# Performance work log

Measured on AMD Instinct MI355X. Metric: run time of the kernel, lower is better.

Reference implementation:

```python
import jax, jax.numpy as jnp
import numpy as np

B, H, S, D = 2, 8, 2048, 64
TEMPERATURE = 8.0  # sqrt(D)

def setup_inputs() -> dict:
    key = jax.random.key(0)
    k1, k2, k3, k4, k5 = jax.random.split(key, 5)
    q = jax.random.normal(k1, (B, H, S, D), dtype=jnp.float32)
    k = jax.random.normal(k2, (B, H, S, D), dtype=jnp.float32)
    v = jax.random.normal(k3, (B, H, S, D), dtype=jnp.float32)
    static_cov = jax.random.normal(k4, (B, S, S), dtype=jnp.float32)
    mask = jax.random.randint(k5, (B, 1, S, S), 0, 2, dtype=jnp.int32)
    # learned parameter: lambda_w initialized to 10 per head, shape [1,H,1,1]
    lambda_w = jnp.full((1, H, 1, 1), 10.0, dtype=jnp.float32)
    return {"q": q, "k": k, "v": v, "static_cov": static_cov,
            "lambda_w": lambda_w, "mask": mask}

def reference(q, k, v, static_cov, lambda_w, mask):
    # blend of scaled QK^T and static covariance bias, convex weights per head
    w_qk = 1.0 / (lambda_w + 1.0)          # [1,H,1,1]
    w_cov = lambda_w / (lambda_w + 1.0)    # [1,H,1,1]
    scores = jnp.einsum('bhsd,bhtd->bhst', q / TEMPERATURE, k)  # [B,H,S,S]
    attn_logits = w_qk * scores + w_cov * static_cov[:, None, :, :]
    attn_logits = jnp.where(mask == 0, jnp.float32(-1e9), attn_logits)
    attn = jax.nn.softmax(attn_logits, axis=-1)  # dropout p=0 -> identity
    output = jnp.einsum('bhst,bhtd->bhsd', attn, v)
    return (output, attn)
```

## Files before the change

kernel.cpp:

```cpp
#include <hip/hip_runtime.h>

#define Bdim 2
#define Hdim 8
#define Sdim 2048
#define Ddim 64
#define PSTR 2056
#define NW 8

typedef short bf16x8 __attribute__((ext_vector_type(8)));
typedef short bf16x4 __attribute__((ext_vector_type(4)));
typedef float f32x4 __attribute__((ext_vector_type(4)));

static __device__ __forceinline__ short f2bf(float x) {
  return __builtin_bit_cast(short, (__bf16)x);
}
static __device__ __forceinline__ float bf2f(short x) {
  unsigned u = ((unsigned)(unsigned short)x) << 16;
  return __builtin_bit_cast(float, u);
}
static __device__ __forceinline__ bf16x8 pack8(float4 a, float4 b, float s) {
  bf16x8 r;
  r[0] = f2bf(a.x * s); r[1] = f2bf(a.y * s);
  r[2] = f2bf(a.z * s); r[3] = f2bf(a.w * s);
  r[4] = f2bf(b.x * s); r[5] = f2bf(b.y * s);
  r[6] = f2bf(b.z * s); r[7] = f2bf(b.w * s);
  return r;
}

__global__ __launch_bounds__(256) void cvt_k(const float* __restrict__ kp,
                                             short* __restrict__ kb) {
  size_t i = ((size_t)blockIdx.x * 256 + threadIdx.x) * 8;
  float4 x0 = *(const float4*)(kp + i);
  float4 x1 = *(const float4*)(kp + i + 4);
  bf16x8 r = pack8(x0, x1, 1.0f);
  *(bf16x8*)(kb + i) = r;
}

__global__ __launch_bounds__(256) void tr_v(const float* __restrict__ vp,
                                            short* __restrict__ vt) {
  __shared__ float tile[64][65];
  const int bh = blockIdx.x >> 5;
  const int t0 = (blockIdx.x & 31) << 6;
  const float* src = vp + ((size_t)bh * Sdim + t0) * Ddim;
  {
    const int tl = threadIdx.x >> 2;
    const int dg = threadIdx.x & 3;
#pragma unroll
    for (int q = 0; q < 4; ++q) {
      float4 x = *(const float4*)(src + tl * Ddim + dg * 16 + q * 4);
      tile[tl][dg * 16 + q * 4 + 0] = x.x;
      tile[tl][dg * 16 + q * 4 + 1] = x.y;
      tile[tl][dg * 16 + q * 4 + 2] = x.z;
      tile[tl][dg * 16 + q * 4 + 3] = x.w;
    }
  }
  __syncthreads();
  {
    const int d  = threadIdx.x >> 2;
    const int tg = threadIdx.x & 3;
    short* dst = vt + ((size_t)bh * Ddim + d) * Sdim + t0 + tg * 16;
    bf16x8 o0, o1;
#pragma unroll
    for (int j = 0; j < 8; ++j) o0[j] = f2bf(tile[tg * 16 + j][d]);
#pragma unroll
    for (int j = 0; j < 8; ++j) o1[j] = f2bf(tile[tg * 16 + 8 + j][d]);
    *(bf16x8*)(dst) = o0;
    *(bf16x8*)(dst + 8) = o1;
  }
}

#define DECLS(S)                                                               \
  bf16x8 kb0a##S, kb0b##S, kb1a##S, kb1b##S;                                   \
  float cv0##S, cv1##S, cv2##S, cv3##S, cv4##S, cv5##S, cv6##S, cv7##S;        \
  int mk0##S, mk1##S, mk2##S, mk3##S, mk4##S, mk5##S, mk6##S, mk7##S;

#define LOADS_KCM(S, T0) {                                                     \
    const int _t = (T0);                                                       \
    kb0a##S = *(const bf16x8*)(kbh + (((size_t)(_t + l15)) << 6) + (quad << 3));        \
    kb0b##S = *(const bf16x8*)(kbh + (((size_t)(_t + l15)) << 6) + (quad << 3) + 32);   \
    kb1a##S = *(const bf16x8*)(kbh + (((size_t)(_t + 16 + l15)) << 6) + (quad << 3));      \
    kb1b##S = *(const bf16x8*)(kbh + (((size_t)(_t + 16 + l15)) << 6) + (quad << 3) + 32); \
    const float* _c = covb + (quad * 4) * Sdim + _t + l15;                     \
    const int*   _m = mb   + (quad * 4) * Sdim + _t + l15;                     \
    cv0##S = _c[0];             mk0##S = _m[0];                                \
    cv1##S = _c[16];            mk1##S = _m[16];                               \
    cv2##S = _c[Sdim];          mk2##S = _m[Sdim];                             \
    cv3##S = _c[Sdim + 16];     mk3##S = _m[Sdim + 16];                        \
    cv4##S = _c[2 * Sdim];      mk4##S = _m[2 * Sdim];                         \
    cv5##S = _c[2 * Sdim + 16]; mk5##S = _m[2 * Sdim + 16];                    \
    cv6##S = _c[3 * Sdim];      mk6##S = _m[3 * Sdim];                         \
    cv7##S = _c[3 * Sdim + 16]; mk7##S = _m[3 * Sdim + 16];                    \
  }

#define LOADS_VB(T0) {                                                         \
    const int _t = (T0);                                                       \
    vb0 = *(const bf16x8*)(vtb + (((size_t)(l15))      << 11) + _t + (quad << 3)); \
    vb1 = *(const bf16x8*)(vtb + (((size_t)(16 + l15)) << 11) + _t + (quad << 3)); \
    vb2 = *(const bf16x8*)(vtb + (((size_t)(32 + l15)) << 11) + _t + (quad << 3)); \
    vb3 = *(const bf16x8*)(vtb + (((size_t)(48 + l15)) << 11) + _t + (quad << 3)); \
  }

#define COMPUTE(S, T0) {                                                       \
    f32x4 a0 = {0.f, 0.f, 0.f, 0.f}, a1 = {0.f, 0.f, 0.f, 0.f};               \
    a0 = __builtin_amdgcn_mfma_f32_16x16x32_bf16(aq0, kb0a##S, a0, 0, 0, 0);   \
    a0 = __builtin_amdgcn_mfma_f32_16x16x32_bf16(aq1, kb0b##S, a0, 0, 0, 0);   \
    a1 = __builtin_amdgcn_mfma_f32_16x16x32_bf16(aq0, kb1a##S, a1, 0, 0, 0);   \
    a1 = __builtin_amdgcn_mfma_f32_16x16x32_bf16(aq1, kb1b##S, a1, 0, 0, 0);   \
    const int col0 = (T0) + l15;                                               \
    const int row0 = quad * 4;                                                 \
    float p;                                                                   \
    p = mk0##S ? __expf(a0[0] + w_cov * cv0##S) : 0.f; lsum[0] += p; Pl[row0 + 0][col0]      = f2bf(p); \
    p = mk1##S ? __expf(a1[0] + w_cov * cv1##S) : 0.f; lsum[0] += p; Pl[row0 + 0][col0 + 16] = f2bf(p); \
    p = mk2##S ? __expf(a0[1] + w_cov * cv2##S) : 0.f; lsum[1] += p; Pl[row0 + 1][col0]      = f2bf(p); \
    p = mk3##S ? __expf(a1[1] + w_cov * cv3##S) : 0.f; lsum[1] += p; Pl[row0 + 1][col0 + 16] = f2bf(p); \
    p = mk4##S ? __expf(a0[2] + w_cov * cv4##S) : 0.f; lsum[2] += p; Pl[row0 + 2][col0]      = f2bf(p); \
    p = mk5##S ? __expf(a1[2] + w_cov * cv5##S) : 0.f; lsum[2] += p; Pl[row0 + 2][col0 + 16] = f2bf(p); \
    p = mk6##S ? __expf(a0[3] + w_cov * cv6##S) : 0.f; lsum[3] += p; Pl[row0 + 3][col0]      = f2bf(p); \
    p = mk7##S ? __expf(a1[3] + w_cov * cv7##S) : 0.f; lsum[3] += p; Pl[row0 + 3][col0 + 16] = f2bf(p); \
    bf16x8 pa = *(const bf16x8*)&Pl[l15][(T0) + quad * 8];                     \
    oacc0 = __builtin_amdgcn_mfma_f32_16x16x32_bf16(pa, vb0, oacc0, 0, 0, 0);  \
    oacc1 = __builtin_amdgcn_mfma_f32_16x16x32_bf16(pa, vb1, oacc1, 0, 0, 0);  \
    oacc2 = __builtin_amdgcn_mfma_f32_16x16x32_bf16(pa, vb2, oacc2, 0, 0, 0);  \
    oacc3 = __builtin_amdgcn_mfma_f32_16x16x32_bf16(pa, vb3, oacc3, 0, 0, 0);  \
  }

__global__ __launch_bounds__(512, 4) void fused_attn(
    const float* __restrict__ qp, const short* __restrict__ kbp,
    const short* __restrict__ vtp, const float* __restrict__ covp,
    const float* __restrict__ lamp, const int* __restrict__ maskp,
    float* __restrict__ outO, float* __restrict__ outA)
{
  __shared__ __align__(16) short Pl[16][PSTR];
  __shared__ float Ls[NW][16];
  __shared__ float Lrow[16];

  const int tid  = threadIdx.x;
  const int wv   = tid >> 6;
  const int lane = tid & 63;
  const int quad = lane >> 4;
  const int l15  = lane & 15;

  const int bid = blockIdx.x;
  const int h  = bid & 7;
  const int qt = (bid >> 3) & 127;
  const int b  = bid >> 10;

  const float lam   = lamp[h];
  const float w_qk  = 1.0f / (lam + 1.0f);
  const float w_cov = lam / (lam + 1.0f);
  const float qscale = w_qk * 0.125f;

  const int q0 = qt * 16;
  const int bh = b * Hdim + h;

  const float* qbase = qp + ((size_t)bh * Sdim + q0) * Ddim;
  const short* kbh   = kbp + (size_t)bh * Sdim * Ddim;
  const short* vtb   = vtp + (size_t)bh * Ddim * Sdim;
  const float* covb  = covp + ((size_t)b * Sdim + q0) * Sdim;
  const int*   mb    = maskp + ((size_t)b * Sdim + q0) * Sdim;
  float* oA = outA + ((size_t)bh * Sdim + q0) * (size_t)Sdim;
  float* oO = outO + ((size_t)bh * Sdim + q0) * Ddim;

  bf16x8 aq0, aq1;
  {
    const float* qr = qbase + l15 * Ddim + quad * 8;
    float4 x0 = *(const float4*)(qr);
    float4 x1 = *(const float4*)(qr + 4);
    aq0 = pack8(x0, x1, qscale);
    float4 y0 = *(const float4*)(qr + 32);
    float4 y1 = *(const float4*)(qr + 36);
    aq1 = pack8(y0, y1, qscale);
  }

  const int tbeg = wv * (Sdim / NW);
  const int tend = tbeg + (Sdim / NW);

  float lsum[4] = {0.f, 0.f, 0.f, 0.f};
  f32x4 oacc0 = {0.f, 0.f, 0.f, 0.f}, oacc1 = {0.f, 0.f, 0.f, 0.f};
  f32x4 oacc2 = {0.f, 0.f, 0.f, 0.f}, oacc3 = {0.f, 0.f, 0.f, 0.f};
  bf16x8 vb0, vb1, vb2, vb3;

  DECLS(E)
  DECLS(O)
  LOADS_KCM(E, tbeg)
#pragma unroll 1
  for (int t0 = tbeg; t0 < tend; t0 += 64) {
    LOADS_VB(t0)
    LOADS_KCM(O, t0 + 32)
    COMPUTE(E, t0)
    const int tnx = (t0 + 64 < tend) ? (t0 + 64) : tbeg;
    LOADS_VB(t0 + 32)
    LOADS_KCM(E, tnx)
    COMPUTE(O, t0 + 32)
  }

#pragma unroll
  for (int r = 0; r < 4; ++r) {
    float s = lsum[r];
    s += __shfl_xor(s, 1, 16);
    s += __shfl_xor(s, 2, 16);
    s += __shfl_xor(s, 4, 16);
    s += __shfl_xor(s, 8, 16);
    if (l15 == 0) Ls[wv][quad * 4 + r] = s;
  }
  __syncthreads();
  if (tid < 16) {
    float s = 0.f;
#pragma unroll
    for (int w2 = 0; w2 < NW; ++w2) s += Ls[w2][tid];
    Lrow[tid] = 1.0f / s;
  }
  __syncthreads();

#pragma unroll 1
  for (int row = 0; row < 16; ++row) {
    const float rinv = Lrow[row];
    float* orow = oA + (size_t)row * Sdim;
    const int c0 = tbeg + lane * 4;
    bf16x4 pv = *(const bf16x4*)&Pl[row][c0];
    f32x4 o;
    o[0] = bf2f(pv[0]) * rinv;
    o[1] = bf2f(pv[1]) * rinv;
    o[2] = bf2f(pv[2]) * rinv;
    o[3] = bf2f(pv[3]) * rinv;
    __builtin_nontemporal_store(o, (f32x4*)&orow[c0]);
  }
  __syncthreads();

  float* Ored = (float*)&Pl[0][0];
#pragma unroll
  for (int r = 0; r < 4; ++r) {
    Ored[((wv * 64 + lane) * 16) + 0  + r] = oacc0[r];
    Ored[((wv * 64 + lane) * 16) + 4  + r] = oacc1[r];
    Ored[((wv * 64 + lane) * 16) + 8  + r] = oacc2[r];
    Ored[((wv * 64 + lane) * 16) + 12 + r] = oacc3[r];
  }
  __syncthreads();
  if (wv < 4) {
#pragma unroll
    for (int r = 0; r < 4; ++r) {
      float s = 0.f;
#pragma unroll
      for (int w2 = 0; w2 < NW; ++w2)
        s += Ored[((w2 * 64 + lane) * 16) + wv * 4 + r];
      const int row = quad * 4 + r;
      __builtin_nontemporal_store(s * Lrow[row], &oO[row * Ddim + wv * 16 + l15]);
    }
  }
}

extern "C" void kernel_launch(void* const* d_in, const int* in_sizes, int n_in,
                              void* d_out, int out_size, void* d_ws, size_t ws_size,
                              hipStream_t stream) {
  const float* q    = (const float*)d_in[0];
  const float* k    = (const float*)d_in[1];
  const float* v    = (const float*)d_in[2];
  const float* cov  = (const float*)d_in[3];
  const float* lam  = (const float*)d_in[4];
  const int*   mask = (const int*)d_in[5];
  float* outO = (float*)d_out;
  float* outA = outO + (size_t)Bdim * Hdim * Sdim * Ddim;

  short* kb = (short*)d_ws;
  short* vt = kb + (size_t)Bdim * Hdim * Sdim * Ddim;
  (void)ws_size;

  cvt_k<<<dim3((Bdim * Hdim * Sdim * Ddim) / (256 * 8)), 256, 0, stream>>>(k, kb);
  tr_v<<<dim3(Bdim * Hdim * (Sdim / 64)), 256, 0, stream>>>(v, vt);

  dim3 grid(Bdim * Hdim * (Sdim / 16));
  fused_attn<<<grid, 512, 0, stream>>>(q, kb, vt, cov, lam, mask, outO, outA);
}
```

Before: 502.8 us.

## Premerge mask into covariance bias in a tiled layout for vectorized loads

Adds a prepass kernel that folds the int mask into the covariance matrix, writing -1e9 where masked. It stores the result in a per-16-row-tile layout of [tile][column][16 rows]. The attention kernel then fetches bias values as two f32x4 vector loads per step instead of eight scalar cov loads plus eight mask loads, and drops the per-element select. The intent is to halve the bias bytes read per head and cut load instruction count. The cost is an extra kernel pass over cov and mask, plus a 32 MB workspace region that must fit within the provided workspace.

```diff
diff --git a/kernel.cpp b/kernel.cpp
--- a/kernel.cpp
+++ b/kernel.cpp
@@ -69,10 +69,28 @@
   }
 }
 
+__global__ __launch_bounds__(256) void cvt_cov(const float* __restrict__ covp,
+                                               const int* __restrict__ maskp,
+                                               float* __restrict__ cm) {
+  const int pair  = blockIdx.x >> 3;
+  const int chunk = blockIdx.x & 7;
+  const int col   = chunk * 256 + threadIdx.x;
+  const size_t rowbase = (size_t)pair * 16;
+  float tmp[16];
+#pragma unroll
+  for (int r = 0; r < 16; ++r) {
+    float c = covp[(rowbase + r) * Sdim + col];
+    int   m = maskp[(rowbase + r) * Sdim + col];
+    tmp[r] = m ? c : -1e9f;
+  }
+  float* dst = cm + ((size_t)pair * Sdim + col) * 16;
+#pragma unroll
+  for (int r = 0; r < 16; ++r) dst[r] = tmp[r];
+}
+
 #define DECLS(S)                                                               \
   bf16x8 kb0a##S, kb0b##S, kb1a##S, kb1b##S;                                   \
-  float cv0##S, cv1##S, cv2##S, cv3##S, cv4##S, cv5##S, cv6##S, cv7##S;        \
-  int mk0##S, mk1##S, mk2##S, mk3##S, mk4##S, mk5##S, mk6##S, mk7##S;
+  f32x4 cva##S, cvb##S;
 
 #define LOADS_KCM(S, T0) {                                                     \
     const int _t = (T0);                                                       \
@@ -80,16 +98,8 @@
     kb0b##S = *(const bf16x8*)(kbh + (((size_t)(_t + l15)) << 6) + (quad << 3) + 32);   \
     kb1a##S = *(const bf16x8*)(kbh + (((size_t)(_t + 16 + l15)) << 6) + (quad << 3));      \
     kb1b##S = *(const bf16x8*)(kbh + (((size_t)(_t + 16 + l15)) << 6) + (quad << 3) + 32); \
-    const float* _c = covb + (quad * 4) * Sdim + _t + l15;                     \
-    const int*   _m = mb   + (quad * 4) * Sdim + _t + l15;                     \
-    cv0##S = _c[0];             mk0##S = _m[0];                                \
-    cv1##S = _c[16];            mk1##S = _m[16];                               \
-    cv2##S = _c[Sdim];          mk2##S = _m[Sdim];                             \
-    cv3##S = _c[Sdim + 16];     mk3##S = _m[Sdim + 16];                        \
-    cv4##S = _c[2 * Sdim];      mk4##S = _m[2 * Sdim];                         \
-    cv5##S = _c[2 * Sdim + 16]; mk5##S = _m[2 * Sdim + 16];                    \
-    cv6##S = _c[3 * Sdim];      mk6##S = _m[3 * Sdim];                         \
-    cv7##S = _c[3 * Sdim + 16]; mk7##S = _m[3 * Sdim + 16];                    \
+    cva##S = *(const f32x4*)(cmb + (((size_t)(_t + l15)) << 4) + (quad << 2));        \
+    cvb##S = *(const f32x4*)(cmb + (((size_t)(_t + 16 + l15)) << 4) + (quad << 2));   \
   }
 
 #define LOADS_VB(T0) {                                                         \
@@ -108,15 +118,13 @@
     a1 = __builtin_amdgcn_mfma_f32_16x16x32_bf16(aq1, kb1b##S, a1, 0, 0, 0);   \
     const int col0 = (T0) + l15;                                               \
     const int row0 = quad * 4;                                                 \
-    float p;                                                                   \
-    p = mk0##S ? __expf(a0[0] + w_cov * cv0##S) : 0.f; lsum[0] += p; Pl[row0 + 0][col0]      = f2bf(p); \
-    p = mk1##S ? __expf(a1[0] + w_cov * cv1##S) : 0.f; lsum[0] += p; Pl[row0 + 0][col0 + 16] = f2bf(p); \
-    p = mk2##S ? __expf(a0[1] + w_cov * cv2##S) : 0.f; lsum[1] += p; Pl[row0 + 1][col0]      = f2bf(p); \
-    p = mk3##S ? __expf(a1[1] + w_cov * cv3##S) : 0.f; lsum[1] += p; Pl[row0 + 1][col0 + 16] = f2bf(p); \
-    p = mk4##S ? __expf(a0[2] + w_cov * cv4##S) : 0.f; lsum[2] += p; Pl[row0 + 2][col0]      = f2bf(p); \
-    p = mk5##S ? __expf(a1[2] + w_cov * cv5##S) : 0.f; lsum[2] += p; Pl[row0 + 2][col0 + 16] = f2bf(p); \
-    p = mk6##S ? __expf(a0[3] + w_cov * cv6##S) : 0.f; lsum[3] += p; Pl[row0 + 3][col0]      = f2bf(p); \
-    p = mk7##S ? __expf(a1[3] + w_cov * cv7##S) : 0.f; lsum[3] += p; Pl[row0 + 3][col0 + 16] = f2bf(p); \
+    _Pragma("unroll") for (int r = 0; r < 4; ++r) {                            \
+      float p0 = __expf(a0[r] + w_cov * cva##S[r]);                            \
+      float p1 = __expf(a1[r] + w_cov * cvb##S[r]);                            \
+      lsum[r] += p0 + p1;                                                      \
+      Pl[row0 + r][col0]      = f2bf(p0);                                      \
+      Pl[row0 + r][col0 + 16] = f2bf(p1);                                      \
+    }                                                                          \
     bf16x8 pa = *(const bf16x8*)&Pl[l15][(T0) + quad * 8];                     \
     oacc0 = __builtin_amdgcn_mfma_f32_16x16x32_bf16(pa, vb0, oacc0, 0, 0, 0);  \
     oacc1 = __builtin_amdgcn_mfma_f32_16x16x32_bf16(pa, vb1, oacc1, 0, 0, 0);  \
@@ -126,8 +134,8 @@
 
 __global__ __launch_bounds__(512, 4) void fused_attn(
     const float* __restrict__ qp, const short* __restrict__ kbp,
-    const short* __restrict__ vtp, const float* __restrict__ covp,
-    const float* __restrict__ lamp, const int* __restrict__ maskp,
+    const short* __restrict__ vtp, const float* __restrict__ cmp,
+    const float* __restrict__ lamp,
     float* __restrict__ outO, float* __restrict__ outA)
 {
   __shared__ __align__(16) short Pl[16][PSTR];
@@ -156,8 +164,7 @@
   const float* qbase = qp + ((size_t)bh * Sdim + q0) * Ddim;
   const short* kbh   = kbp + (size_t)bh * Sdim * Ddim;
   const short* vtb   = vtp + (size_t)bh * Ddim * Sdim;
-  const float* covb  = covp + ((size_t)b * Sdim + q0) * Sdim;
-  const int*   mb    = maskp + ((size_t)b * Sdim + q0) * Sdim;
+  const float* cmb   = cmp + ((size_t)(b * 128 + qt)) * Sdim * 16;
   float* oA = outA + ((size_t)bh * Sdim + q0) * (size_t)Sdim;
   float* oO = outO + ((size_t)bh * Sdim + q0) * Ddim;
 
@@ -263,11 +270,13 @@
 
   short* kb = (short*)d_ws;
   short* vt = kb + (size_t)Bdim * Hdim * Sdim * Ddim;
+  float* cm = (float*)(vt + (size_t)Bdim * Hdim * Sdim * Ddim);
   (void)ws_size;
 
   cvt_k<<<dim3((Bdim * Hdim * Sdim * Ddim) / (256 * 8)), 256, 0, stream>>>(k, kb);
   tr_v<<<dim3(Bdim * Hdim * (Sdim / 64)), 256, 0, stream>>>(v, vt);
+  cvt_cov<<<dim3(Bdim * (Sdim / 16) * 8), 256, 0, stream>>>(cov, mask, cm);
 
   dim3 grid(Bdim * Hdim * (Sdim / 16));
-  fused_attn<<<grid, 512, 0, stream>>>(q, kb, vt, cov, lam, mask, outO, outA);
-}
+  fused_attn<<<grid, 512, 0, stream>>>(q, kb, vt, cm, lam, outO, outA);
+}
```

After: 468.5 us. 1.07x faster.
